# Kernel tuning notes

Measured on AMD Instinct MI355X. Metric: run time of the kernel, lower is better.

Reference implementation:

```python
import jax, jax.numpy as jnp
import numpy as np
import math

NBITS = (1, 2, 4, 8)
S, B, D, H, F = 1024, 8, 1024, 16, 4096
HD = D // H


def _quant(w, nbit):
    """Symmetric uniform weight quantization to `nbit` bits with STE."""
    if nbit == 1:
        q = jnp.sign(w) * jnp.mean(jnp.abs(w))
    else:
        qmax = float(2 ** (nbit - 1) - 1)
        scale = jnp.max(jnp.abs(w)) / qmax
        q = jnp.clip(jnp.round(w / scale), -qmax - 1.0, qmax) * scale
    # straight-through estimator: forward uses q, backward flows through w
    return w + jax.lax.stop_gradient(q - w)


def _layernorm(x, g, b, eps=1e-5):
    m = jnp.mean(x, axis=-1, keepdims=True)
    v = jnp.var(x, axis=-1, keepdims=True)
    return (x - m) * jax.lax.rsqrt(v + eps) * g + b


def _quant_attn(src, w_in, b_in, w_out, b_out, nbit):
    # src: [S,B,D]; w_in: [3D,D]; w_out: [D,D]
    w_in_q = _quant(w_in, nbit)
    w_out_q = _quant(w_out, nbit)
    qkv = jnp.einsum('sbd,ed->sbe', src, w_in_q) + b_in  # [S,B,3D]
    q, k, v = jnp.split(qkv, 3, axis=-1)
    q = q.reshape(S, B, H, HD)
    k = k.reshape(S, B, H, HD)
    v = v.reshape(S, B, H, HD)
    scores = jnp.einsum('sbhd,tbhd->bhst', q, k) * (1.0 / math.sqrt(HD))
    p = jax.nn.softmax(scores, axis=-1)  # [B,H,S,S]
    o = jnp.einsum('bhst,tbhd->sbhd', p, v).reshape(S, B, D)
    return jnp.einsum('sbd,ed->sbe', o, w_out_q) + b_out


def setup_inputs() -> dict:
    key = jax.random.key(0)
    ks = jax.random.split(key, 12)
    sc = 0.02
    return {
        'src': jax.random.normal(ks[0], (S, B, D), jnp.float32),
        'alpha': jax.random.normal(ks[1], (3, 4), jnp.float32),
        'in_proj_w': jax.random.normal(ks[2], (4, 3 * D, D), jnp.float32) * sc,
        'in_proj_b': jnp.zeros((4, 3 * D), jnp.float32),
        'out_proj_w': jax.random.normal(ks[3], (4, D, D), jnp.float32) * sc,
        'out_proj_b': jnp.zeros((4, D), jnp.float32),
        'w1': jax.random.normal(ks[4], (4, F, D), jnp.float32) * sc,
        'b1': jnp.zeros((4, F), jnp.float32),
        'w2': jax.random.normal(ks[5], (4, D, F), jnp.float32) * sc,
        'b2': jnp.zeros((4, D), jnp.float32),
        'g1': jnp.ones((D,), jnp.float32),
        'be1': jnp.zeros((D,), jnp.float32),
        'g2': jnp.ones((D,), jnp.float32),
        'be2': jnp.zeros((D,), jnp.float32),
    }


def reference(src, alpha, in_proj_w, in_proj_b, out_proj_w, out_proj_b,
              w1, b1, w2, b2, g1, be1, g2, be2):
    probs = jax.nn.softmax(alpha, axis=-1)  # [3,4]
    # softmax-weighted mixture of multi-bitwidth attention branches
    src2 = jnp.zeros_like(src)
    for i, nbit in enumerate(NBITS):
        src2 = src2 + probs[0, i] * _quant_attn(
            src, in_proj_w[i], in_proj_b[i], out_proj_w[i], out_proj_b[i], nbit)
    x = _layernorm(src + src2, g1, be1)
    # mixture of quantized linear1 branches, then GELU
    h = jnp.zeros((S, B, F), src.dtype)
    for i, nbit in enumerate(NBITS):
        h = h + probs[1, i] * (jnp.einsum('sbd,fd->sbf', x, _quant(w1[i], nbit)) + b1[i])
    h = jax.nn.gelu(h, approximate=False)
    # mixture of quantized linear2 branches
    y = jnp.zeros_like(x)
    for i, nbit in enumerate(NBITS):
        y = y + probs[2, i] * (jnp.einsum('sbf,df->sbd', h, _quant(w2[i], nbit)) + b2[i])
    return _layernorm(x + y, g2, be2)
```

## Files before the change

kernel.cpp:

```cpp
#include <hip/hip_runtime.h>
#include <hip/hip_bf16.h>

typedef __attribute__((ext_vector_type(8))) unsigned short u16x8;
typedef __attribute__((ext_vector_type(4))) unsigned short u16x4;
typedef __attribute__((ext_vector_type(4))) int            i32x4;
typedef __attribute__((ext_vector_type(8))) __bf16         bf16x8;
typedef __attribute__((ext_vector_type(4))) float          f32x4;

#define SS 1024
#define BB 8
#define DD 1024
#define HH 16
#define HDD 64
#define FF 4096
#define MM 8192

#define GL16(g, l) __builtin_amdgcn_global_load_lds( \
    (__attribute__((address_space(1))) const void*)(g), \
    (__attribute__((address_space(3))) void*)(l), 16, 0, 0)

__device__ __forceinline__ float bf2f(unsigned short u) {
    return __uint_as_float(((unsigned int)u) << 16);
}
__device__ __forceinline__ unsigned short f2bf(float f) {
    unsigned int u = __float_as_uint(f);
    unsigned int r = (u + 0x7fffu + ((u >> 16) & 1u)) >> 16;
    return (unsigned short)r;
}
__device__ __forceinline__ float quantv(float w, float som, float qm) {
    if (qm == 0.f) {
        float sgn = (w > 0.f) ? 1.f : ((w < 0.f) ? -1.f : 0.f);
        return sgn * som;
    }
    if (som == 0.f) return 0.f;
    float q = rintf(w / som);
    q = fminf(fmaxf(q, -qm - 1.f), qm);
    return q * som;
}

__global__ __launch_bounds__(256) void k_stats(const float* __restrict__ w_in, const float* __restrict__ w_out,
                                               const float* __restrict__ w1, const float* __restrict__ w2,
                                               const float* __restrict__ src,
                                               float* __restrict__ pmax, float* __restrict__ psum) {
    const int t = blockIdx.y, blk = blockIdx.x, tid = threadIdx.x;
    const float* base; int n;
    if (t < 4)       { base = w_in  + (size_t)t * 3145728;     n = 3145728; }
    else if (t < 8)  { base = w_out + (size_t)(t-4) * 1048576; n = 1048576; }
    else if (t < 12) { base = w1    + (size_t)(t-8) * 4194304; n = 4194304; }
    else if (t < 16) { base = w2    + (size_t)(t-12) * 4194304; n = 4194304; }
    else             { base = src;                             n = 8388608; }
    const int n4 = n >> 2;
    float vmax = 0.f, vsum = 0.f;
    for (int i = blk * 256 + tid; i < n4; i += 65536) {
        float4 v = reinterpret_cast<const float4*>(base)[i];
        float a0 = fabsf(v.x), a1 = fabsf(v.y), a2 = fabsf(v.z), a3 = fabsf(v.w);
        vmax = fmaxf(vmax, fmaxf(fmaxf(a0, a1), fmaxf(a2, a3)));
        vsum += (a0 + a1) + (a2 + a3);
    }
#pragma unroll
    for (int m = 1; m < 64; m <<= 1) { vmax = fmaxf(vmax, __shfl_xor(vmax, m, 64)); vsum += __shfl_xor(vsum, m, 64); }
    __shared__ float sm[4], su[4];
    const int wave = tid >> 6, lane = tid & 63;
    if (lane == 0) { sm[wave] = vmax; su[wave] = vsum; }
    __syncthreads();
    if (tid == 0) {
        pmax[t * 256 + blk] = fmaxf(fmaxf(sm[0], sm[1]), fmaxf(sm[2], sm[3]));
        psum[t * 256 + blk] = (su[0] + su[1]) + (su[2] + su[3]);
    }
}

__global__ __launch_bounds__(256) void k_params(const float* __restrict__ pmax, const float* __restrict__ psum,
                                                const float* __restrict__ alpha, float* __restrict__ P) {
    __shared__ float rm[256], rs[256];
    const int tid = threadIdx.x;
    for (int t = 0; t < 17; ++t) {
        rm[tid] = pmax[t * 256 + tid];
        rs[tid] = psum[t * 256 + tid];
        __syncthreads();
        for (int s = 128; s > 0; s >>= 1) {
            if (tid < s) { rm[tid] = fmaxf(rm[tid], rm[tid + s]); rs[tid] += rs[tid + s]; }
            __syncthreads();
        }
        if (tid == 0) {
            if (t == 16) {
                P[50] = rm[0] * (1.f / 127.f);
            } else {
                const int nbits[4] = {1, 2, 4, 8};
                const int nb = nbits[t & 3];
                float nsize = (t < 4) ? 3145728.f : ((t < 8) ? 1048576.f : 4194304.f);
                if (nb == 1) { P[16 + 2*t] = rs[0] / nsize; P[17 + 2*t] = 0.f; }
                else { float qm = (float)((1 << (nb - 1)) - 1); P[16 + 2*t] = rm[0] / qm; P[17 + 2*t] = qm; }
            }
        }
        __syncthreads();
    }
    if (tid < 3) {
        float a[4], mx = -1e30f;
#pragma unroll
        for (int i = 0; i < 4; ++i) { a[i] = alpha[tid * 4 + i]; mx = fmaxf(mx, a[i]); }
        float e[4], ssum = 0.f;
#pragma unroll
        for (int i = 0; i < 4; ++i) { e[i] = expf(a[i] - mx); ssum += e[i]; }
#pragma unroll
        for (int i = 0; i < 4; ++i) P[tid * 4 + i] = e[i] / ssum;
    }
}

__global__ __launch_bounds__(256) void k_quant8(const float* __restrict__ w, signed char* __restrict__ out,
                                                const float* __restrict__ P, int per_tensor, int tbase, int ntot) {
    int i = blockIdx.x * 256 + threadIdx.x;
    if (i >= ntot) return;
    int t = tbase + i / per_tensor;
    float som = P[16 + 2*t], qm = P[17 + 2*t];
    float v;
    float x = w[i];
    if (qm == 0.f)      v = (x > 0.f) ? 1.f : ((x < 0.f) ? -1.f : 0.f);
    else if (som == 0.f) v = 0.f;
    else                v = fminf(fmaxf(rintf(x / som), -qm - 1.f), qm);
    out[i] = (signed char)(int)v;
}

__global__ __launch_bounds__(256) void k_si8(const float* __restrict__ in, signed char* __restrict__ out,
                                             const float* __restrict__ P, int n4) {
    int i = blockIdx.x * 256 + threadIdx.x;
    if (i >= n4) return;
    const float sa = P[50];
    const float inv = (sa > 0.f) ? 1.f / sa : 0.f;
    float4 v = reinterpret_cast<const float4*>(in)[i];
    char4 o;
    o.x = (signed char)(int)fminf(fmaxf(rintf(v.x * inv), -127.f), 127.f);
    o.y = (signed char)(int)fminf(fmaxf(rintf(v.y * inv), -127.f), 127.f);
    o.z = (signed char)(int)fminf(fmaxf(rintf(v.z * inv), -127.f), 127.f);
    o.w = (signed char)(int)fminf(fmaxf(rintf(v.w * inv), -127.f), 127.f);
    reinterpret_cast<char4*>(out)[i] = o;
}

__global__ __launch_bounds__(256) void k_qcat(const float* __restrict__ w_out, unsigned short* __restrict__ out,
                                              const float* __restrict__ P) {
    int j = blockIdx.x * 256 + threadIdx.x;
    if (j >= 4194304) return;
    int d = j >> 12, rr = j & 4095, i = rr >> 10, e = rr & 1023;
    int t = 4 + i;
    float v = quantv(w_out[((size_t)i << 20) + d * 1024 + e], P[16 + 2*t], P[17 + 2*t]);
    out[j] = f2bf(P[i] * v);
}

__global__ __launch_bounds__(256) void k_mix(const float* __restrict__ w, unsigned short* __restrict__ out,
                                             const float* __restrict__ P, int tbase, int prow, int sz) {
    int i = blockIdx.x * 256 + threadIdx.x;
    if (i >= sz) return;
    float acc = 0.f;
#pragma unroll
    for (int br = 0; br < 4; ++br) {
        int t = tbase + br;
        acc += P[prow * 4 + br] * quantv(w[(size_t)br * sz + i], P[16 + 2*t], P[17 + 2*t]);
    }
    out[i] = f2bf(acc);
}
__global__ __launch_bounds__(256) void k_mixb(const float* __restrict__ b, float* __restrict__ out,
                                              const float* __restrict__ P, int prow, int n) {
    int i = blockIdx.x * 256 + threadIdx.x;
    if (i >= n) return;
    float acc = 0.f;
#pragma unroll
    for (int br = 0; br < 4; ++br) acc += P[prow * 4 + br] * b[(size_t)br * n + i];
    out[i] = acc;
}

__device__ __forceinline__ void store_out(float* C, size_t idx, float v) { C[idx] = v; }
__device__ __forceinline__ void store_out(unsigned short* C, size_t idx, float v) { C[idx] = f2bf(v); }

template <typename OutT, bool GELU>
__global__ __launch_bounds__(256) void k_gemm_bt(const unsigned short* __restrict__ A,
                                                 const unsigned short* __restrict__ Bw,
                                                 OutT* __restrict__ C,
                                                 const float* __restrict__ bias,
                                                 int M, int N, int K, int XM, int XN) {
    const int gx = gridDim.x, gy = gridDim.y;
    const int flat = blockIdx.x + gx * blockIdx.y;
    const int xcd = flat & 7, r = flat >> 3;
    const int nloc = gx / XN, mloc = gy / XM;
    const int cm = xcd / XN, cn = xcd - cm * XN;
    const int by = cm * mloc + r / nloc;
    const int bx = cn * nloc + (r - (r / nloc) * nloc);

    __shared__ unsigned short As[2][128 * 64];
    __shared__ unsigned short Bs[2][128 * 64];
    const int tid = threadIdx.x;
    const int m0 = by * 128, n0 = bx * 128;
    const int lane = tid & 63, wave = tid >> 6;
    const int wr = wave >> 1, wc = wave & 1;
    const int lr = lane & 15, lg = lane >> 4;
    const int rsub = lane >> 3;
    const int csub = ((lane & 7) ^ rsub) * 8;
    const size_t aoff = (size_t)(m0 + rsub) * K + csub;
    const size_t boff = (size_t)(n0 + rsub) * K + csub;

    f32x4 acc[4][4];
#pragma unroll
    for (int m = 0; m < 4; ++m)
#pragma unroll
        for (int n = 0; n < 4; ++n) acc[m][n] = (f32x4){0.f, 0.f, 0.f, 0.f};

    auto stage = [&](int buf, int k0) {
#pragma unroll
        for (int it = 0; it < 4; ++it) {
            const int g = it * 4 + wave;
            GL16(A + aoff + (size_t)g * 8 * K + k0, &As[buf][g * 512]);
            GL16(Bw + boff + (size_t)g * 8 * K + k0, &Bs[buf][g * 512]);
        }
    };
    auto compute = [&](int buf) {
#pragma unroll
        for (int kh = 0; kh < 2; ++kh) {
            u16x8 af[4], bfr[4];
#pragma unroll
            for (int m = 0; m < 4; ++m) {
                int row = wr * 64 + m * 16 + lr;
                int cidx = (kh * 4 + lg) ^ (lr & 7);
                af[m] = *reinterpret_cast<const u16x8*>(&As[buf][row * 64 + cidx * 8]);
            }
#pragma unroll
            for (int n = 0; n < 4; ++n) {
                int row = wc * 64 + n * 16 + lr;
                int cidx = (kh * 4 + lg) ^ (lr & 7);
                bfr[n] = *reinterpret_cast<const u16x8*>(&Bs[buf][row * 64 + cidx * 8]);
            }
#pragma unroll
            for (int m = 0; m < 4; ++m)
#pragma unroll
                for (int n = 0; n < 4; ++n)
                    acc[m][n] = __builtin_amdgcn_mfma_f32_16x16x32_bf16(
                        __builtin_bit_cast(bf16x8, af[m]), __builtin_bit_cast(bf16x8, bfr[n]),
                        acc[m][n], 0, 0, 0);
        }
    };

    stage(0, 0);
    __syncthreads();
    int cur = 0;
    for (int k0 = 64; k0 < K; k0 += 64) {
        stage(cur ^ 1, k0);
        compute(cur);
        __syncthreads();
        cur ^= 1;
    }
    compute(cur);

#pragma unroll
    for (int n = 0; n < 4; ++n) {
        const int col = n0 + wc * 64 + n * 16 + lr;
        const float bv = bias ? bias[col] : 0.f;
#pragma unroll
        for (int m = 0; m < 4; ++m) {
#pragma unroll
            for (int j = 0; j < 4; ++j) {
                const int row = m0 + wr * 64 + m * 16 + lg * 4 + j;
                float v = acc[m][n][j] + bv;
                if (GELU) v = 0.5f * v * (1.f + erff(v * 0.70710678118654752f));
                store_out(C, (size_t)row * N + col, v);
            }
        }
    }
}

__global__ __launch_bounds__(256) void k_gemm_i8(const signed char* __restrict__ A,
                                                 const signed char* __restrict__ Bw,
                                                 unsigned short* __restrict__ C,
                                                 const float* __restrict__ bias,
                                                 const float* __restrict__ P, int tIdx,
                                                 int M, int N, int K, int XM, int XN) {
    const int gx = gridDim.x, gy = gridDim.y;
    const int flat = blockIdx.x + gx * blockIdx.y;
    const int xcd = flat & 7, r = flat >> 3;
    const int nloc = gx / XN, mloc = gy / XM;
    const int cm = xcd / XN, cn = xcd - cm * XN;
    const int by = cm * mloc + r / nloc;
    const int bx = cn * nloc + (r - (r / nloc) * nloc);

    __shared__ signed char As[2][128 * 128];
    __shared__ signed char Bs[2][128 * 128];
    const int tid = threadIdx.x;
    const int m0 = by * 128, n0 = bx * 128;
    const int lane = tid & 63, wave = tid >> 6;
    const int wr = wave >> 1, wc = wave & 1;
    const int lr = lane & 15, lg = lane >> 4;
    const int rsub = lane >> 3;
    const int csub = ((lane & 7) ^ rsub) * 16;
    const size_t aoff = (size_t)(m0 + rsub) * K + csub;
    const size_t boff = (size_t)(n0 + rsub) * K + csub;

    i32x4 acc[4][4];
#pragma unroll
    for (int m = 0; m < 4; ++m)
#pragma unroll
        for (int n = 0; n < 4; ++n) acc[m][n] = (i32x4){0, 0, 0, 0};

    auto stage = [&](int buf, int k0) {
#pragma unroll
        for (int it = 0; it < 4; ++it) {
            const int g = it * 4 + wave;
            GL16(A + aoff + (size_t)g * 8 * K + k0, &As[buf][g * 1024]);
            GL16(Bw + boff + (size_t)g * 8 * K + k0, &Bs[buf][g * 1024]);
        }
    };
    auto compute = [&](int buf) {
#pragma unroll
        for (int kh = 0; kh < 2; ++kh) {
            i32x4 af[4], bfr[4];
#pragma unroll
            for (int m = 0; m < 4; ++m) {
                int row = wr * 64 + m * 16 + lr;
                int cidx = (kh * 4 + lg) ^ (lr & 7);
                af[m] = *reinterpret_cast<const i32x4*>(&As[buf][row * 128 + cidx * 16]);
            }
#pragma unroll
            for (int n = 0; n < 4; ++n) {
                int row = wc * 64 + n * 16 + lr;
                int cidx = (kh * 4 + lg) ^ (lr & 7);
                bfr[n] = *reinterpret_cast<const i32x4*>(&Bs[buf][row * 128 + cidx * 16]);
            }
#pragma unroll
            for (int m = 0; m < 4; ++m)
#pragma unroll
                for (int n = 0; n < 4; ++n)
                    acc[m][n] = __builtin_amdgcn_mfma_i32_16x16x64_i8(
                        af[m], bfr[n], acc[m][n], 0, 0, 0);
        }
    };

    stage(0, 0);
    __syncthreads();
    int cur = 0;
    for (int k0 = 128; k0 < K; k0 += 128) {
        stage(cur ^ 1, k0);
        compute(cur);
        __syncthreads();
        cur ^= 1;
    }
    compute(cur);

    const float sab = P[50] * P[16 + 2 * tIdx];
#pragma unroll
    for (int n = 0; n < 4; ++n) {
        const int col = n0 + wc * 64 + n * 16 + lr;
        const float bv = bias[col];
#pragma unroll
        for (int m = 0; m < 4; ++m) {
#pragma unroll
            for (int j = 0; j < 4; ++j) {
                const int row = m0 + wr * 64 + m * 16 + lg * 4 + j;
                float v = (float)acc[m][n][j] * sab + bv;
                C[(size_t)row * N + col] = f2bf(v);
            }
        }
    }
}

__global__ __launch_bounds__(256) void k_fmfma(const unsigned short* __restrict__ qkvb, int qstride,
                                               unsigned short* __restrict__ outb, int ostride) {
    __shared__ unsigned short Ks[64 * 64];
    __shared__ unsigned short Vt[64 * 64];
    __shared__ unsigned short Pl[4 * 16 * 72];
    const int tid = threadIdx.x;
    const int lane = tid & 63, wave = tid >> 6;
    const int lr = lane & 15, lg = lane >> 4;
    const int s0 = blockIdx.x * 64;
    const int bh = blockIdx.y;
    const int b = bh >> 4, hh = bh & 15;
    const int hb = hh * 64;

    u16x8 qf[2];
    {
        const size_t qb = (size_t)((s0 + wave * 16 + lr) * 8 + b) * qstride + hb;
#pragma unroll
        for (int ks = 0; ks < 2; ++ks)
            qf[ks] = *reinterpret_cast<const u16x8*>(qkvb + qb + ks * 32 + lg * 8);
    }
    float m_old = -1e30f, l_run = 0.f;
    f32x4 oacc[4];
#pragma unroll
    for (int n = 0; n < 4; ++n) oacc[n] = (f32x4){0.f, 0.f, 0.f, 0.f};
    unsigned short* myP = Pl + wave * (16 * 72);

    for (int kt = 0; kt < 16; ++kt) {
        __syncthreads();
#pragma unroll
        for (int it = 0; it < 2; ++it) {
            int c = tid + it * 256;
            int row = c >> 3, ch = c & 7;
            const size_t gb = (size_t)((kt * 64 + row) * 8 + b) * qstride + hb + ch * 8;
            int chs = ch ^ (row & 7);
            *reinterpret_cast<u16x8*>(&Ks[row * 64 + chs * 8]) =
                *reinterpret_cast<const u16x8*>(qkvb + gb + 1024);
            u16x8 vv = *reinterpret_cast<const u16x8*>(qkvb + gb + 2048);
            const int vbase = ((row >> 3) ^ ch) * 8 + (row & 7);
#pragma unroll
            for (int e = 0; e < 8; ++e) Vt[(ch * 8 + e) * 64 + vbase] = vv[e];
        }
        __syncthreads();
        f32x4 sacc[4];
#pragma unroll
        for (int n = 0; n < 4; ++n) sacc[n] = (f32x4){0.f, 0.f, 0.f, 0.f};
#pragma unroll
        for (int ks = 0; ks < 2; ++ks) {
#pragma unroll
            for (int n = 0; n < 4; ++n) {
                int row = n * 16 + lr;
                int cidx = (ks * 4 + lg) ^ (lr & 7);
                u16x8 kf = *reinterpret_cast<const u16x8*>(&Ks[row * 64 + cidx * 8]);
                sacc[n] = __builtin_amdgcn_mfma_f32_16x16x32_bf16(
                    __builtin_bit_cast(bf16x8, kf), __builtin_bit_cast(bf16x8, qf[ks]),
                    sacc[n], 0, 0, 0);
            }
        }
        float pmax = -1e30f;
#pragma unroll
        for (int n = 0; n < 4; ++n)
#pragma unroll
            for (int j = 0; j < 4; ++j) { sacc[n][j] *= 0.125f; pmax = fmaxf(pmax, sacc[n][j]); }
        pmax = fmaxf(pmax, __shfl_xor(pmax, 16, 64));
        pmax = fmaxf(pmax, __shfl_xor(pmax, 32, 64));
        const float m_new = fmaxf(m_old, pmax);
        const float corr = __expf(m_old - m_new);
        float pv[16];
        float psum = 0.f;
#pragma unroll
        for (int n = 0; n < 4; ++n)
#pragma unroll
            for (int j = 0; j < 4; ++j) { float e = __expf(sacc[n][j] - m_new); pv[n * 4 + j] = e; psum += e; }
        psum += __shfl_xor(psum, 16, 64);
        psum += __shfl_xor(psum, 32, 64);
        l_run = l_run * corr + psum;
        m_old = m_new;
#pragma unroll
        for (int n = 0; n < 4; ++n)
#pragma unroll
            for (int t2 = 0; t2 < 2; ++t2) {
                int key = n * 16 + lg * 4 + t2 * 2;
                unsigned int pk = (unsigned int)f2bf(pv[n * 4 + t2 * 2]) |
                                  ((unsigned int)f2bf(pv[n * 4 + t2 * 2 + 1]) << 16);
                *reinterpret_cast<unsigned int*>(&myP[lr * 72 + key]) = pk;
            }
#pragma unroll
        for (int j = 0; j < 4; ++j) {
            float cj = __shfl(corr, lg * 4 + j, 64);
#pragma unroll
            for (int n = 0; n < 4; ++n) oacc[n][j] *= cj;
        }
#pragma unroll
        for (int ks = 0; ks < 2; ++ks) {
            u16x8 pa = *reinterpret_cast<const u16x8*>(&myP[lr * 72 + ks * 32 + lg * 8]);
#pragma unroll
            for (int n = 0; n < 4; ++n) {
                int d = n * 16 + lr;
                int kcs = (ks * 4 + lg) ^ (d >> 3);
                u16x8 vf = *reinterpret_cast<const u16x8*>(&Vt[d * 64 + kcs * 8]);
                oacc[n] = __builtin_amdgcn_mfma_f32_16x16x32_bf16(
                    __builtin_bit_cast(bf16x8, pa), __builtin_bit_cast(bf16x8, vf),
                    oacc[n], 0, 0, 0);
            }
        }
    }
    const float linv = 1.f / l_run;
#pragma unroll
    for (int j = 0; j < 4; ++j) {
        float lj = __shfl(linv, lg * 4 + j, 64);
        const size_t rowb = (size_t)((s0 + wave * 16 + lg * 4 + j) * 8 + b) * ostride + hb;
#pragma unroll
        for (int n = 0; n < 4; ++n)
            outb[rowb + n * 16 + lr] = f2bf(oacc[n][j] * lj);
    }
}

__global__ __launch_bounds__(256) void k_ln(const float* __restrict__ xf, const unsigned short* __restrict__ xb,
                                            const float* __restrict__ r,
                                            const float* __restrict__ g, const float* __restrict__ be,
                                            float* __restrict__ outf, unsigned short* __restrict__ outb) {
    const int row = blockIdx.x, tid = threadIdx.x;
    const size_t base = (size_t)row * 1024 + tid * 4;
    float x0, x1, x2, x3;
    if (xf) {
        float4 xv = *reinterpret_cast<const float4*>(xf + base);
        x0 = xv.x; x1 = xv.y; x2 = xv.z; x3 = xv.w;
    } else {
        u16x4 xv = *reinterpret_cast<const u16x4*>(xb + base);
        x0 = bf2f(xv[0]); x1 = bf2f(xv[1]); x2 = bf2f(xv[2]); x3 = bf2f(xv[3]);
    }
    float4 rv = *reinterpret_cast<const float4*>(r + base);
    float t0 = x0 + rv.x, t1 = x1 + rv.y, t2 = x2 + rv.z, t3 = x3 + rv.w;
    float s = t0 + t1 + t2 + t3;
    float ss = t0 * t0 + t1 * t1 + t2 * t2 + t3 * t3;
#pragma unroll
    for (int m = 1; m < 64; m <<= 1) { s += __shfl_xor(s, m, 64); ss += __shfl_xor(ss, m, 64); }
    __shared__ float red[8];
    const int wave = tid >> 6, lane = tid & 63;
    if (lane == 0) { red[wave] = s; red[4 + wave] = ss; }
    __syncthreads();
    s = red[0] + red[1] + red[2] + red[3];
    ss = red[4] + red[5] + red[6] + red[7];
    const float mean = s * (1.f / 1024.f);
    const float var = ss * (1.f / 1024.f) - mean * mean;
    const float rstd = rsqrtf(var + 1e-5f);
    float4 gv = *reinterpret_cast<const float4*>(g + tid * 4);
    float4 bv = *reinterpret_cast<const float4*>(be + tid * 4);
    float o0 = (t0 - mean) * rstd * gv.x + bv.x;
    float o1 = (t1 - mean) * rstd * gv.y + bv.y;
    float o2 = (t2 - mean) * rstd * gv.z + bv.z;
    float o3 = (t3 - mean) * rstd * gv.w + bv.w;
    if (outf) {
        float4 ov = {o0, o1, o2, o3};
        *reinterpret_cast<float4*>(outf + base) = ov;
    }
    if (outb) {
        u16x4 q; q[0] = f2bf(o0); q[1] = f2bf(o1); q[2] = f2bf(o2); q[3] = f2bf(o3);
        *reinterpret_cast<u16x4*>(outb + base) = q;
    }
}

extern "C" void kernel_launch(void* const* d_in, const int* in_sizes, int n_in,
                              void* d_out, int out_size, void* d_ws, size_t ws_size,
                              hipStream_t stream) {
    const float* src   = (const float*)d_in[0];
    const float* alpha = (const float*)d_in[1];
    const float* w_in  = (const float*)d_in[2];
    const float* b_in  = (const float*)d_in[3];
    const float* w_out = (const float*)d_in[4];
    const float* b_out = (const float*)d_in[5];
    const float* w1    = (const float*)d_in[6];
    const float* b1    = (const float*)d_in[7];
    const float* w2    = (const float*)d_in[8];
    const float* b2    = (const float*)d_in[9];
    const float* g1    = (const float*)d_in[10];
    const float* be1   = (const float*)d_in[11];
    const float* g2    = (const float*)d_in[12];
    const float* be2   = (const float*)d_in[13];

    char* ws = (char*)d_ws;
    size_t off = 0;
    auto alloc = [&](size_t bytes) { size_t r = off; off += (bytes + 255) & ~(size_t)255; return r; };
    float* P              = (float*)(ws + alloc(1024));
    float* pmax           = (float*)(ws + alloc(17 * 256 * 4));
    float* psum           = (float*)(ws + alloc(17 * 256 * 4));
    signed char* WinQ8    = (signed char*)(ws + alloc((size_t)4 * 3072 * 1024));
    unsigned short* WoutC = (unsigned short*)(ws + alloc((size_t)1024 * 4096 * 2));
    unsigned short* W1m   = (unsigned short*)(ws + alloc((size_t)4096 * 1024 * 2));
    unsigned short* W2m   = (unsigned short*)(ws + alloc((size_t)1024 * 4096 * 2));
    float* b1m            = (float*)(ws + alloc(4096 * 4));
    float* b2m            = (float*)(ws + alloc(1024 * 4));
    float* bOm            = (float*)(ws + alloc(1024 * 4));
    signed char* Si8      = (signed char*)(ws + alloc((size_t)MM * 1024));
    unsigned short* Xbf   = (unsigned short*)(ws + alloc((size_t)MM * 1024 * 2));
    unsigned short* attnC = (unsigned short*)(ws + alloc((size_t)MM * 4096 * 2));
    unsigned short* qkvB  = (unsigned short*)(ws + alloc((size_t)MM * 3072 * 2));
    unsigned short* h     = attnC;
    if (ws_size < off) return;

    float* outF = (float*)d_out;

    k_stats<<<dim3(256, 17), 256, 0, stream>>>(w_in, w_out, w1, w2, src, pmax, psum);
    k_params<<<1, 256, 0, stream>>>(pmax, psum, alpha, P);
    {
        int n = 4 * 3072 * 1024;
        k_quant8<<<(n + 255) / 256, 256, 0, stream>>>(w_in, WinQ8, P, 3072 * 1024, 0, n);
        k_qcat<<<(4194304 + 255) / 256, 256, 0, stream>>>(w_out, WoutC, P);
        n = 4096 * 1024;
        k_mix<<<(n + 255) / 256, 256, 0, stream>>>(w1, W1m, P, 8, 1, n);
        k_mix<<<(n + 255) / 256, 256, 0, stream>>>(w2, W2m, P, 12, 2, n);
        k_mixb<<<(4096 + 255) / 256, 256, 0, stream>>>(b1, b1m, P, 1, 4096);
        k_mixb<<<(1024 + 255) / 256, 256, 0, stream>>>(b2, b2m, P, 2, 1024);
        k_mixb<<<(1024 + 255) / 256, 256, 0, stream>>>(b_out, bOm, P, 0, 1024);
        k_si8<<<(2097152 + 255) / 256, 256, 0, stream>>>(src, Si8, P, 2097152);
    }
    for (int i = 0; i < 4; ++i) {
        k_gemm_i8<<<dim3(24, 64), 256, 0, stream>>>(
            Si8, WinQ8 + (size_t)i * 3072 * 1024, qkvB, b_in + i * 3072, P, i, MM, 3072, 1024, 1, 8);
        k_fmfma<<<dim3(16, 128), 256, 0, stream>>>(qkvB, 3072, attnC + i * 1024, 4096);
    }
    k_gemm_bt<float, false><<<dim3(8, 64), 256, 0, stream>>>(
        attnC, WoutC, outF, bOm, MM, 1024, 4096, 4, 2);
    k_ln<<<MM, 256, 0, stream>>>(src, nullptr, outF, g1, be1, nullptr, Xbf);
    k_gemm_bt<unsigned short, true><<<dim3(32, 64), 256, 0, stream>>>(
        Xbf, W1m, h, b1m, MM, 4096, 1024, 1, 8);
    k_gemm_bt<float, false><<<dim3(8, 64), 256, 0, stream>>>(
        h, W2m, outF, b2m, MM, 1024, 4096, 4, 2);
    k_ln<<<MM, 256, 0, stream>>>(nullptr, Xbf, outF, g2, be2, outF, nullptr);
}
```

Measured before the change: 995.1 us.

## Move out-proj and FFN GEMMs to int8 MFMA with dynamic per-tensor activation scales

The bf16 GEMMs for the output projection, linear1 and linear2 become int8 GEMMs using the 16x16x64 i8 MFMA. Mixed weights are requantized per row to int8 with a per-row scale. Activations get a per-tensor absmax, gathered by atomicMax in the attention, LayerNorm and GEMM epilogues, and are quantized by a separate pass. The aim is to double matrix-core throughput and halve operand traffic, at the cost of extra quantization passes and notable accuracy loss on activations.

```diff
diff --git a/kernel.cpp b/kernel.cpp
--- a/kernel.cpp
+++ b/kernel.cpp
@@ -135,28 +135,48 @@
     reinterpret_cast<char4*>(out)[i] = o;
 }
 
-__global__ __launch_bounds__(256) void k_qcat(const float* __restrict__ w_out, unsigned short* __restrict__ out,
-                                              const float* __restrict__ P) {
-    int j = blockIdx.x * 256 + threadIdx.x;
-    if (j >= 4194304) return;
-    int d = j >> 12, rr = j & 4095, i = rr >> 10, e = rr & 1023;
-    int t = 4 + i;
-    float v = quantv(w_out[((size_t)i << 20) + d * 1024 + e], P[16 + 2*t], P[17 + 2*t]);
-    out[j] = f2bf(P[i] * v);
-}
-
-__global__ __launch_bounds__(256) void k_mix(const float* __restrict__ w, unsigned short* __restrict__ out,
-                                             const float* __restrict__ P, int tbase, int prow, int sz) {
-    int i = blockIdx.x * 256 + threadIdx.x;
-    if (i >= sz) return;
-    float acc = 0.f;
-#pragma unroll
-    for (int br = 0; br < 4; ++br) {
-        int t = tbase + br;
-        acc += P[prow * 4 + br] * quantv(w[(size_t)br * sz + i], P[16 + 2*t], P[17 + 2*t]);
-    }
-    out[i] = f2bf(acc);
-}
+template <int NE, int MODE>
+__global__ __launch_bounds__(256) void k_mixq8(const float* __restrict__ w, signed char* __restrict__ out,
+                                               float* __restrict__ sB, const float* __restrict__ P,
+                                               int tbase, int prow, size_t sz) {
+    const int row = blockIdx.x, tid = threadIdx.x;
+    const int L = NE * 256;
+    float v[NE];
+    float lm = 0.f;
+#pragma unroll
+    for (int j = 0; j < NE; ++j) {
+        int k = j * 256 + tid;
+        float acc;
+        if (MODE == 0) {
+            acc = 0.f;
+#pragma unroll
+            for (int br = 0; br < 4; ++br) {
+                int t = tbase + br;
+                acc += P[prow * 4 + br] * quantv(w[(size_t)br * sz + (size_t)row * L + k], P[16 + 2*t], P[17 + 2*t]);
+            }
+        } else {
+            int i = k >> 10, e = k & 1023;
+            int t = tbase + i;
+            acc = P[i] * quantv(w[(size_t)i * sz + (size_t)row * 1024 + e], P[16 + 2*t], P[17 + 2*t]);
+        }
+        v[j] = acc;
+        lm = fmaxf(lm, fabsf(acc));
+    }
+#pragma unroll
+    for (int m = 1; m < 64; m <<= 1) lm = fmaxf(lm, __shfl_xor(lm, m, 64));
+    __shared__ float sm[4];
+    const int wave = tid >> 6, lane = tid & 63;
+    if (lane == 0) sm[wave] = lm;
+    __syncthreads();
+    lm = fmaxf(fmaxf(sm[0], sm[1]), fmaxf(sm[2], sm[3]));
+    if (tid == 0) sB[row] = lm * (1.f / 127.f);
+    const float inv = (lm > 0.f) ? 127.f / lm : 0.f;
+#pragma unroll
+    for (int j = 0; j < NE; ++j)
+        out[(size_t)row * L + j * 256 + tid] =
+            (signed char)(int)fminf(fmaxf(rintf(v[j] * inv), -127.f), 127.f);
+}
+
 __global__ __launch_bounds__(256) void k_mixb(const float* __restrict__ b, float* __restrict__ out,
                                               const float* __restrict__ P, int prow, int n) {
     int i = blockIdx.x * 256 + threadIdx.x;
@@ -167,101 +187,20 @@
     out[i] = acc;
 }
 
-__device__ __forceinline__ void store_out(float* C, size_t idx, float v) { C[idx] = v; }
-__device__ __forceinline__ void store_out(unsigned short* C, size_t idx, float v) { C[idx] = f2bf(v); }
-
-template <typename OutT, bool GELU>
-__global__ __launch_bounds__(256) void k_gemm_bt(const unsigned short* __restrict__ A,
-                                                 const unsigned short* __restrict__ Bw,
-                                                 OutT* __restrict__ C,
-                                                 const float* __restrict__ bias,
-                                                 int M, int N, int K, int XM, int XN) {
-    const int gx = gridDim.x, gy = gridDim.y;
-    const int flat = blockIdx.x + gx * blockIdx.y;
-    const int xcd = flat & 7, r = flat >> 3;
-    const int nloc = gx / XN, mloc = gy / XM;
-    const int cm = xcd / XN, cn = xcd - cm * XN;
-    const int by = cm * mloc + r / nloc;
-    const int bx = cn * nloc + (r - (r / nloc) * nloc);
-
-    __shared__ unsigned short As[2][128 * 64];
-    __shared__ unsigned short Bs[2][128 * 64];
-    const int tid = threadIdx.x;
-    const int m0 = by * 128, n0 = bx * 128;
-    const int lane = tid & 63, wave = tid >> 6;
-    const int wr = wave >> 1, wc = wave & 1;
-    const int lr = lane & 15, lg = lane >> 4;
-    const int rsub = lane >> 3;
-    const int csub = ((lane & 7) ^ rsub) * 8;
-    const size_t aoff = (size_t)(m0 + rsub) * K + csub;
-    const size_t boff = (size_t)(n0 + rsub) * K + csub;
-
-    f32x4 acc[4][4];
-#pragma unroll
-    for (int m = 0; m < 4; ++m)
-#pragma unroll
-        for (int n = 0; n < 4; ++n) acc[m][n] = (f32x4){0.f, 0.f, 0.f, 0.f};
-
-    auto stage = [&](int buf, int k0) {
-#pragma unroll
-        for (int it = 0; it < 4; ++it) {
-            const int g = it * 4 + wave;
-            GL16(A + aoff + (size_t)g * 8 * K + k0, &As[buf][g * 512]);
-            GL16(Bw + boff + (size_t)g * 8 * K + k0, &Bs[buf][g * 512]);
-        }
-    };
-    auto compute = [&](int buf) {
-#pragma unroll
-        for (int kh = 0; kh < 2; ++kh) {
-            u16x8 af[4], bfr[4];
-#pragma unroll
-            for (int m = 0; m < 4; ++m) {
-                int row = wr * 64 + m * 16 + lr;
-                int cidx = (kh * 4 + lg) ^ (lr & 7);
-                af[m] = *reinterpret_cast<const u16x8*>(&As[buf][row * 64 + cidx * 8]);
-            }
-#pragma unroll
-            for (int n = 0; n < 4; ++n) {
-                int row = wc * 64 + n * 16 + lr;
-                int cidx = (kh * 4 + lg) ^ (lr & 7);
-                bfr[n] = *reinterpret_cast<const u16x8*>(&Bs[buf][row * 64 + cidx * 8]);
-            }
-#pragma unroll
-            for (int m = 0; m < 4; ++m)
-#pragma unroll
-                for (int n = 0; n < 4; ++n)
-                    acc[m][n] = __builtin_amdgcn_mfma_f32_16x16x32_bf16(
-                        __builtin_bit_cast(bf16x8, af[m]), __builtin_bit_cast(bf16x8, bfr[n]),
-                        acc[m][n], 0, 0, 0);
-        }
-    };
-
-    stage(0, 0);
-    __syncthreads();
-    int cur = 0;
-    for (int k0 = 64; k0 < K; k0 += 64) {
-        stage(cur ^ 1, k0);
-        compute(cur);
-        __syncthreads();
-        cur ^= 1;
-    }
-    compute(cur);
-
-#pragma unroll
-    for (int n = 0; n < 4; ++n) {
-        const int col = n0 + wc * 64 + n * 16 + lr;
-        const float bv = bias ? bias[col] : 0.f;
-#pragma unroll
-        for (int m = 0; m < 4; ++m) {
-#pragma unroll
-            for (int j = 0; j < 4; ++j) {
-                const int row = m0 + wr * 64 + m * 16 + lg * 4 + j;
-                float v = acc[m][n][j] + bv;
-                if (GELU) v = 0.5f * v * (1.f + erff(v * 0.70710678118654752f));
-                store_out(C, (size_t)row * N + col, v);
-            }
-        }
-    }
+__global__ __launch_bounds__(256) void k_q8(const unsigned short* __restrict__ in, signed char* __restrict__ out,
+                                            const unsigned* __restrict__ amax, int n8) {
+    int i = blockIdx.x * 256 + threadIdx.x;
+    if (i >= n8) return;
+    const float am = __uint_as_float(*amax);
+    const float inv = (am > 0.f) ? 127.f / am : 0.f;
+    u16x8 v = reinterpret_cast<const u16x8*>(in)[i];
+    union { signed char c[8]; unsigned long long u; } r;
+#pragma unroll
+    for (int e = 0; e < 8; ++e) {
+        float f = bf2f(v[e]) * inv;
+        r.c[e] = (signed char)(int)fminf(fmaxf(rintf(f), -127.f), 127.f);
+    }
+    reinterpret_cast<unsigned long long*>(out)[i] = r.u;
 }
 
 __global__ __launch_bounds__(256) void k_gemm_i8(const signed char* __restrict__ A,
@@ -357,8 +296,117 @@
     }
 }
 
+__device__ __forceinline__ void store_out(float* C, size_t idx, float v) { C[idx] = v; }
+__device__ __forceinline__ void store_out(unsigned short* C, size_t idx, float v) { C[idx] = f2bf(v); }
+
+template <typename OutT, bool GELU>
+__global__ __launch_bounds__(256) void k_gemm_i8s(const signed char* __restrict__ A,
+                                                  const signed char* __restrict__ Bw,
+                                                  OutT* __restrict__ C,
+                                                  const float* __restrict__ bias,
+                                                  const float* __restrict__ sB,
+                                                  const unsigned* __restrict__ aAmax,
+                                                  unsigned* oAmax,
+                                                  int M, int N, int K, int XM, int XN) {
+    const int gx = gridDim.x, gy = gridDim.y;
+    const int flat = blockIdx.x + gx * blockIdx.y;
+    const int xcd = flat & 7, r = flat >> 3;
+    const int nloc = gx / XN, mloc = gy / XM;
+    const int cm = xcd / XN, cn = xcd - cm * XN;
+    const int by = cm * mloc + r / nloc;
+    const int bx = cn * nloc + (r - (r / nloc) * nloc);
+
+    __shared__ signed char As[2][128 * 128];
+    __shared__ signed char Bs[2][128 * 128];
+    const int tid = threadIdx.x;
+    const int m0 = by * 128, n0 = bx * 128;
+    const int lane = tid & 63, wave = tid >> 6;
+    const int wr = wave >> 1, wc = wave & 1;
+    const int lr = lane & 15, lg = lane >> 4;
+    const int rsub = lane >> 3;
+    const int csub = ((lane & 7) ^ rsub) * 16;
+    const size_t aoff = (size_t)(m0 + rsub) * K + csub;
+    const size_t boff = (size_t)(n0 + rsub) * K + csub;
+
+    i32x4 acc[4][4];
+#pragma unroll
+    for (int m = 0; m < 4; ++m)
+#pragma unroll
+        for (int n = 0; n < 4; ++n) acc[m][n] = (i32x4){0, 0, 0, 0};
+
+    auto stage = [&](int buf, int k0) {
+#pragma unroll
+        for (int it = 0; it < 4; ++it) {
+            const int g = it * 4 + wave;
+            GL16(A + aoff + (size_t)g * 8 * K + k0, &As[buf][g * 1024]);
+            GL16(Bw + boff + (size_t)g * 8 * K + k0, &Bs[buf][g * 1024]);
+        }
+    };
+    auto compute = [&](int buf) {
+#pragma unroll
+        for (int kh = 0; kh < 2; ++kh) {
+            i32x4 af[4], bfr[4];
+#pragma unroll
+            for (int m = 0; m < 4; ++m) {
+                int row = wr * 64 + m * 16 + lr;
+                int cidx = (kh * 4 + lg) ^ (lr & 7);
+                af[m] = *reinterpret_cast<const i32x4*>(&As[buf][row * 128 + cidx * 16]);
+            }
+#pragma unroll
+            for (int n = 0; n < 4; ++n) {
+                int row = wc * 64 + n * 16 + lr;
+                int cidx = (kh * 4 + lg) ^ (lr & 7);
+                bfr[n] = *reinterpret_cast<const i32x4*>(&Bs[buf][row * 128 + cidx * 16]);
+            }
+#pragma unroll
+            for (int m = 0; m < 4; ++m)
+#pragma unroll
+                for (int n = 0; n < 4; ++n)
+                    acc[m][n] = __builtin_amdgcn_mfma_i32_16x16x64_i8(
+                        af[m], bfr[n], acc[m][n], 0, 0, 0);
+        }
+    };
+
+    stage(0, 0);
+    __syncthreads();
+    int cur = 0;
+    for (int k0 = 128; k0 < K; k0 += 128) {
+        stage(cur ^ 1, k0);
+        compute(cur);
+        __syncthreads();
+        cur ^= 1;
+    }
+    compute(cur);
+
+    const float sA = __uint_as_float(*aAmax) * (1.f / 127.f);
+    float lm = 0.f;
+#pragma unroll
+    for (int n = 0; n < 4; ++n) {
+        const int col = n0 + wc * 64 + n * 16 + lr;
+        const float sc = sA * sB[col];
+        const float bv = bias ? bias[col] : 0.f;
+#pragma unroll
+        for (int m = 0; m < 4; ++m) {
+#pragma unroll
+            for (int j = 0; j < 4; ++j) {
+                const int row = m0 + wr * 64 + m * 16 + lg * 4 + j;
+                float v = (float)acc[m][n][j] * sc + bv;
+                if (GELU) v = 0.5f * v * (1.f + erff(v * 0.70710678118654752f));
+                store_out(C, (size_t)row * N + col, v);
+                if (oAmax) lm = fmaxf(lm, fabsf(v));
+            }
+        }
+    }
+    if (oAmax) {
+#pragma unroll
+        for (int m = 1; m < 64; m <<= 1) lm = fmaxf(lm, __shfl_xor(lm, m, 64));
+        if (lane == 0) atomicMax(oAmax, __float_as_uint(lm));
+    }
+}
+
 __global__ __launch_bounds__(256) void k_fmfma(const unsigned short* __restrict__ qkvb, int qstride,
-                                               unsigned short* __restrict__ outb, int ostride) {
+                                               unsigned short* __restrict__ outb, int ostride,
+                                               unsigned* __restrict__ oAmax) {
     __shared__ unsigned short Ks[64 * 64];
     __shared__ unsigned short Vt[64 * 64];
     __shared__ unsigned short Pl[4 * 16 * 72];
@@ -463,20 +511,28 @@
         }
     }
     const float linv = 1.f / l_run;
+    float lm = 0.f;
 #pragma unroll
     for (int j = 0; j < 4; ++j) {
         float lj = __shfl(linv, lg * 4 + j, 64);
         const size_t rowb = (size_t)((s0 + wave * 16 + lg * 4 + j) * 8 + b) * ostride + hb;
 #pragma unroll
-        for (int n = 0; n < 4; ++n)
-            outb[rowb + n * 16 + lr] = f2bf(oacc[n][j] * lj);
-    }
+        for (int n = 0; n < 4; ++n) {
+            float v = oacc[n][j] * lj;
+            outb[rowb + n * 16 + lr] = f2bf(v);
+            lm = fmaxf(lm, fabsf(v));
+        }
+    }
+#pragma unroll
+    for (int m = 1; m < 64; m <<= 1) lm = fmaxf(lm, __shfl_xor(lm, m, 64));
+    if (lane == 0) atomicMax(oAmax, __float_as_uint(lm));
 }
 
 __global__ __launch_bounds__(256) void k_ln(const float* __restrict__ xf, const unsigned short* __restrict__ xb,
                                             const float* __restrict__ r,
                                             const float* __restrict__ g, const float* __restrict__ be,
-                                            float* __restrict__ outf, unsigned short* __restrict__ outb) {
+                                            float* __restrict__ outf, unsigned short* __restrict__ outb,
+                                            unsigned* __restrict__ oAmax) {
     const int row = blockIdx.x, tid = threadIdx.x;
     const size_t base = (size_t)row * 1024 + tid * 4;
     float x0, x1, x2, x3;
@@ -516,6 +572,12 @@
         u16x4 q; q[0] = f2bf(o0); q[1] = f2bf(o1); q[2] = f2bf(o2); q[3] = f2bf(o3);
         *reinterpret_cast<u16x4*>(outb + base) = q;
     }
+    if (oAmax) {
+        float lm = fmaxf(fmaxf(fabsf(o0), fabsf(o1)), fmaxf(fabsf(o2), fabsf(o3)));
+#pragma unroll
+        for (int m = 1; m < 64; m <<= 1) lm = fmaxf(lm, __shfl_xor(lm, m, 64));
+        if (lane == 0) atomicMax(oAmax, __float_as_uint(lm));
+    }
 }
 
 extern "C" void kernel_launch(void* const* d_in, const int* in_sizes, int n_in,
@@ -540,33 +602,40 @@
     size_t off = 0;
     auto alloc = [&](size_t bytes) { size_t r = off; off += (bytes + 255) & ~(size_t)255; return r; };
     float* P              = (float*)(ws + alloc(1024));
+    unsigned* amax        = (unsigned*)(ws + alloc(256));
     float* pmax           = (float*)(ws + alloc(17 * 256 * 4));
     float* psum           = (float*)(ws + alloc(17 * 256 * 4));
     signed char* WinQ8    = (signed char*)(ws + alloc((size_t)4 * 3072 * 1024));
-    unsigned short* WoutC = (unsigned short*)(ws + alloc((size_t)1024 * 4096 * 2));
-    unsigned short* W1m   = (unsigned short*)(ws + alloc((size_t)4096 * 1024 * 2));
-    unsigned short* W2m   = (unsigned short*)(ws + alloc((size_t)1024 * 4096 * 2));
+    signed char* WoutC8   = (signed char*)(ws + alloc((size_t)1024 * 4096));
+    float* sOut           = (float*)(ws + alloc(1024 * 4));
+    signed char* W1m8     = (signed char*)(ws + alloc((size_t)4096 * 1024));
+    float* s1             = (float*)(ws + alloc(4096 * 4));
+    signed char* W2m8     = (signed char*)(ws + alloc((size_t)1024 * 4096));
+    float* s2             = (float*)(ws + alloc(1024 * 4));
     float* b1m            = (float*)(ws + alloc(4096 * 4));
     float* b2m            = (float*)(ws + alloc(1024 * 4));
     float* bOm            = (float*)(ws + alloc(1024 * 4));
     signed char* Si8      = (signed char*)(ws + alloc((size_t)MM * 1024));
     unsigned short* Xbf   = (unsigned short*)(ws + alloc((size_t)MM * 1024 * 2));
+    signed char* Xi8      = (signed char*)(ws + alloc((size_t)MM * 1024));
     unsigned short* attnC = (unsigned short*)(ws + alloc((size_t)MM * 4096 * 2));
     unsigned short* qkvB  = (unsigned short*)(ws + alloc((size_t)MM * 3072 * 2));
+    signed char* attnC8   = (signed char*)qkvB;
     unsigned short* h     = attnC;
+    signed char* h8       = (signed char*)qkvB;
     if (ws_size < off) return;
 
     float* outF = (float*)d_out;
 
+    hipMemsetAsync(amax, 0, 16, stream);
     k_stats<<<dim3(256, 17), 256, 0, stream>>>(w_in, w_out, w1, w2, src, pmax, psum);
     k_params<<<1, 256, 0, stream>>>(pmax, psum, alpha, P);
     {
         int n = 4 * 3072 * 1024;
         k_quant8<<<(n + 255) / 256, 256, 0, stream>>>(w_in, WinQ8, P, 3072 * 1024, 0, n);
-        k_qcat<<<(4194304 + 255) / 256, 256, 0, stream>>>(w_out, WoutC, P);
-        n = 4096 * 1024;
-        k_mix<<<(n + 255) / 256, 256, 0, stream>>>(w1, W1m, P, 8, 1, n);
-        k_mix<<<(n + 255) / 256, 256, 0, stream>>>(w2, W2m, P, 12, 2, n);
+        k_mixq8<16, 1><<<1024, 256, 0, stream>>>(w_out, WoutC8, sOut, P, 4, 0, 1048576);
+        k_mixq8<4, 0><<<4096, 256, 0, stream>>>(w1, W1m8, s1, P, 8, 1, 4194304);
+        k_mixq8<16, 0><<<1024, 256, 0, stream>>>(w2, W2m8, s2, P, 12, 2, 4194304);
         k_mixb<<<(4096 + 255) / 256, 256, 0, stream>>>(b1, b1m, P, 1, 4096);
         k_mixb<<<(1024 + 255) / 256, 256, 0, stream>>>(b2, b2m, P, 2, 1024);
         k_mixb<<<(1024 + 255) / 256, 256, 0, stream>>>(b_out, bOm, P, 0, 1024);
@@ -575,14 +644,17 @@
     for (int i = 0; i < 4; ++i) {
         k_gemm_i8<<<dim3(24, 64), 256, 0, stream>>>(
             Si8, WinQ8 + (size_t)i * 3072 * 1024, qkvB, b_in + i * 3072, P, i, MM, 3072, 1024, 1, 8);
-        k_fmfma<<<dim3(16, 128), 256, 0, stream>>>(qkvB, 3072, attnC + i * 1024, 4096);
-    }
-    k_gemm_bt<float, false><<<dim3(8, 64), 256, 0, stream>>>(
-        attnC, WoutC, outF, bOm, MM, 1024, 4096, 4, 2);
-    k_ln<<<MM, 256, 0, stream>>>(src, nullptr, outF, g1, be1, nullptr, Xbf);
-    k_gemm_bt<unsigned short, true><<<dim3(32, 64), 256, 0, stream>>>(
-        Xbf, W1m, h, b1m, MM, 4096, 1024, 1, 8);
-    k_gemm_bt<float, false><<<dim3(8, 64), 256, 0, stream>>>(
-        h, W2m, outF, b2m, MM, 1024, 4096, 4, 2);
-    k_ln<<<MM, 256, 0, stream>>>(nullptr, Xbf, outF, g2, be2, outF, nullptr);
-}
+        k_fmfma<<<dim3(16, 128), 256, 0, stream>>>(qkvB, 3072, attnC + i * 1024, 4096, amax + 0);
+    }
+    k_q8<<<(4194304 + 255) / 256, 256, 0, stream>>>(attnC, attnC8, amax + 0, 4194304);
+    k_gemm_i8s<float, false><<<dim3(8, 64), 256, 0, stream>>>(
+        attnC8, WoutC8, outF, bOm, sOut, amax + 0, nullptr, MM, 1024, 4096, 4, 2);
+    k_ln<<<MM, 256, 0, stream>>>(src, nullptr, outF, g1, be1, nullptr, Xbf, amax + 1);
+    k_q8<<<(1048576 + 255) / 256, 256, 0, stream>>>(Xbf, Xi8, amax + 1, 1048576);
+    k_gemm_i8s<unsigned short, true><<<dim3(32, 64), 256, 0, stream>>>(
+        Xi8, W1m8, h, b1m, s1, amax + 1, amax + 2, MM, 4096, 1024, 1, 8);
+    k_q8<<<(4194304 + 255) / 256, 256, 0, stream>>>(h, h8, amax + 2, 4194304);
+    k_gemm_i8s<float, false><<<dim3(8, 64), 256, 0, stream>>>(
+        h8, W2m8, outF, b2m, s2, amax + 2, nullptr, MM, 1024, 4096, 4, 2);
+    k_ln<<<MM, 256, 0, stream>>>(nullptr, Xbf, outF, g2, be2, outF, nullptr, nullptr);
+}
```

New measurement: 1.524 ms. 1.53x slower.
